# Kernel tuning notes

Measured on AMD Instinct MI355X. Metric: run time of the kernel, lower is better.

## Reference

```python
import jax, jax.numpy as jnp
import numpy as np

B, CIN, F, H, W = 4, 256, 128, 64, 64
EPS = 1e-5

def _conv1x1(x, Wm, b):
    # x: [B,C,H,W], Wm: [O,C] (1x1 conv kernel), b: [O]
    return jnp.einsum('bchw,oc->bohw', x, Wm) + b[None, :, None, None]

def setup_inputs() -> dict:
    key = jax.random.key(0)
    ks = jax.random.split(key, 11)
    s_in = 1.0 / np.sqrt(CIN)
    s_f = 1.0 / np.sqrt(F)
    return {
        'x':    jax.random.normal(ks[0], (B, CIN, H, W), jnp.float32),
        'Wg':   jax.random.normal(ks[1], (F, CIN), jnp.float32) * s_in,
        'bg':   jax.random.normal(ks[2], (F,), jnp.float32) * s_in,
        'Wt':   jax.random.normal(ks[3], (F, CIN), jnp.float32) * s_in,
        'bt':   jax.random.normal(ks[4], (F,), jnp.float32) * s_in,
        'Wp':   jax.random.normal(ks[5], (F, CIN), jnp.float32) * s_in,
        'bp':   jax.random.normal(ks[6], (F,), jnp.float32) * s_in,
        'Wz':   jax.random.normal(ks[7], (CIN, F), jnp.float32) * s_f,
        'bz':   jax.random.normal(ks[8], (CIN,), jnp.float32) * s_f,
        'ln_w': jax.random.normal(ks[9], (CIN, H, W), jnp.float32) * 0.1,
        'ln_b': jax.random.normal(ks[10], (CIN, H, W), jnp.float32) * 0.1,
    }

def reference(x, Wg, bg, Wt, bt, Wp, bp, Wz, bz, ln_w, ln_b):
    b, _, h, w = x.shape
    n = h * w
    # 1x1 conv projections
    g = _conv1x1(x, Wg, bg).reshape(b, F, n).transpose(0, 2, 1)      # [B,N,F]
    theta = _conv1x1(x, Wt, bt).reshape(b, F, n).transpose(0, 2, 1)  # [B,N,F]
    phi = _conv1x1(x, Wp, bp).reshape(b, F, n)                        # [B,F,N]
    # embedded-Gaussian affinity + softmax attention
    f = jnp.einsum('bnf,bfm->bnm', theta, phi)                        # [B,N,N]
    attn = jax.nn.softmax(f, axis=-1)
    y = jnp.einsum('bnm,bmf->bnf', attn, g)                           # [B,N,F]
    y = y.transpose(0, 2, 1).reshape(b, F, h, w)                      # [B,F,H,W]
    # output projection
    z = _conv1x1(y, Wz, bz)                                           # [B,CIN,H,W]
    # LayerNorm over (C,H,W) per sample, affine params shaped [C,H,W]
    mu = jnp.mean(z, axis=(1, 2, 3), keepdims=True)
    var = jnp.var(z, axis=(1, 2, 3), keepdims=True)
    z = (z - mu) * jax.lax.rsqrt(var + EPS)
    z = z * ln_w[None] + ln_b[None]
    return z + x
```

## Files before the change

### kernel.cpp

```cpp
#include <hip/hip_runtime.h>
#include <stdint.h>

#define CIN 256
#define FDIM 128
#define NSP 4096
#define EPS 1e-5f

typedef __attribute__((ext_vector_type(8))) short short8;
typedef __attribute__((ext_vector_type(4))) float f32x4;
typedef __attribute__((ext_vector_type(16))) float f32x16;

__device__ __forceinline__ short f2bf(float f) {
  union { float f; uint32_t u; } v; v.f = f;
  uint32_t r = v.u + 0x7fffu + ((v.u >> 16) & 1u);
  return (short)(r >> 16);
}
__device__ __forceinline__ float bf2f(short h) {
  union { uint32_t u; float f; } v; v.u = ((uint32_t)(uint16_t)h) << 16;
  return v.f;
}

__global__ void prep_w(const float* __restrict__ Wg, const float* __restrict__ Wt,
                       const float* __restrict__ Wp, const float* __restrict__ Wz,
                       short* __restrict__ Wbf, short* __restrict__ Wzbf,
                       float* __restrict__ sums) {
  int u = blockIdx.x * 256 + threadIdx.x;
  if (u < 8 && blockIdx.x == 0) sums[u] = 0.f;
  if (u < 12288) {
    int p = u >> 12;
    int rem = u & 4095;
    int ftg = rem >> 9, s = (rem >> 6) & 7, lane = rem & 63;
    int row = ftg * 16 + (lane & 15);
    int col = s * 32 + (lane >> 4) * 8;
    const float* Wsrc = (p == 0) ? Wt : (p == 1) ? Wp : Wg;
    short8 v8;
#pragma unroll
    for (int j = 0; j < 8; j++) v8[j] = f2bf(Wsrc[row * 256 + col + j]);
    *(short8*)(Wbf + (size_t)u * 8) = v8;
  } else if (u < 12288 + 4096) {
    int u2 = u - 12288;
    int cog = u2 >> 8, s = (u2 >> 6) & 3, lane = u2 & 63;
    int co = cog * 16 + (lane & 15);
    int ch = s * 32 + (lane >> 4) * 8;
    short8 v8;
#pragma unroll
    for (int j = 0; j < 8; j++) v8[j] = f2bf(Wz[co * 128 + ch + j]);
    *(short8*)(Wzbf + (size_t)u2 * 8) = v8;
  }
}

__global__ void __launch_bounds__(256)
proj_kernel(const float* __restrict__ x, const short* __restrict__ Wbf,
            const float* __restrict__ bt, const float* __restrict__ bp,
            const float* __restrict__ bg,
            short* __restrict__ theta, short* __restrict__ Kb, short* __restrict__ gT) {
  __shared__ float tile[32][33];
  __shared__ short Axy[32 * 264];
  __shared__ short lds[5120];
  int bx = blockIdx.x;
  int b = bx >> 7;
  int n0 = (bx & 127) << 5;
  int t = threadIdx.x, w = t >> 6, lane = t & 63, l15 = lane & 15, quad = lane >> 4;
  int r = t >> 5, cc = t & 31;

  const float* xb = x + (size_t)b * CIN * NSP;
#pragma unroll
  for (int ch = 0; ch < 8; ch++) {
    int c0 = ch * 32;
#pragma unroll
    for (int k = 0; k < 4; k++)
      tile[r + 8 * k][cc] = xb[(size_t)(c0 + r + 8 * k) * NSP + n0 + cc];
    __syncthreads();
#pragma unroll
    for (int k = 0; k < 4; k++)
      Axy[(r + 8 * k) * 264 + c0 + cc] = f2bf(tile[cc][r + 8 * k]);
    __syncthreads();
  }

  short8 a[8];
  int ar = (w & 1) * 16 + l15;
#pragma unroll
  for (int s = 0; s < 8; s++)
    a[s] = *(const short8*)(Axy + ar * 264 + s * 32 + quad * 8);

  for (int p = 0; p < 3; p++) {
    const short* Wsrc = Wbf + p * 32768;
    f32x4 zero = {0.f, 0.f, 0.f, 0.f};
    f32x4 acc[4];
#pragma unroll
    for (int i = 0; i < 4; i++) acc[i] = zero;

#pragma unroll
    for (int s = 0; s < 8; s++) {
#pragma unroll
      for (int ft = 0; ft < 4; ft++) {
        int ftg = (w >> 1) * 4 + ft;
        short8 bfr = *(const short8*)(Wsrc + (ftg * 8 + s) * 512 + lane * 8);
        acc[ft] = __builtin_amdgcn_mfma_f32_16x16x32_bf16(a[s], bfr, acc[ft], 0, 0, 0);
      }
    }

    const float* bias = (p == 0) ? bt : (p == 1) ? bp : bg;
    if (p > 0) __syncthreads();
    if (p < 2) {
#pragma unroll
      for (int ft = 0; ft < 4; ft++) {
        int ftg = (w >> 1) * 4 + ft;
        float bv = bias[ftg * 16 + l15];
#pragma unroll
        for (int rr = 0; rr < 4; rr++) {
          int n = (w & 1) * 16 + quad * 4 + rr;
          lds[n * 136 + ftg * 16 + l15] = f2bf(acc[ft][rr] + bv);
        }
      }
      __syncthreads();
      short* dst = ((p == 0) ? theta : Kb) + (size_t)(b * NSP + n0) * FDIM;
#pragma unroll
      for (int i = 0; i < 2; i++) {
        int flat = t + 256 * i;
        int row = flat >> 4, ch = flat & 15;
        *(short8*)(dst + (size_t)row * FDIM + ch * 8) = *(const short8*)(lds + row * 136 + ch * 8);
      }
    } else {
#pragma unroll
      for (int ft = 0; ft < 4; ft++) {
        int ftg = (w >> 1) * 4 + ft;
        float bv = bias[ftg * 16 + l15];
#pragma unroll
        for (int rr = 0; rr < 4; rr++) {
          int n = (w & 1) * 16 + quad * 4 + rr;
          lds[(ftg * 16 + l15) * 40 + n] = f2bf(acc[ft][rr] + bv);
        }
      }
      __syncthreads();
      short* dst = gT + (size_t)b * FDIM * NSP + n0;
#pragma unroll
      for (int i = 0; i < 2; i++) {
        int flat = t + 256 * i;
        int f = flat >> 2, c = flat & 3;
        *(short8*)(dst + (size_t)f * NSP + c * 8) = *(const short8*)(lds + f * 40 + c * 8);
      }
    }
  }
}

__global__ void __launch_bounds__(256, 2)
flash_kernel(const short* __restrict__ thetab, const short* __restrict__ Kb,
             const short* __restrict__ gT, short* __restrict__ opart,
             float* __restrict__ lpart) {
  __shared__ __attribute__((aligned(16))) char smem[34816];
  short* Klds = (short*)smem;
  short* Vlds = (short*)(smem + 16384);

  const int bx = blockIdx.x;
  const int b  = bx >> 7;
  const int r  = bx & 127;
  const int q0 = (r >> 2) << 7;
  const int kc = r & 3;
  const int t = threadIdx.x, w = t >> 6, lane = t & 63;
  const int l31 = lane & 31, h = lane >> 5;
  const int qw = q0 + w * 32;

  const short* Qsrc = thetab + (size_t)b * NSP * FDIM;
  const short* Ksrc = Kb + (size_t)b * NSP * FDIM;
  const short* Vsrc = gT + (size_t)b * FDIM * NSP;

  short8 qf[8];
#pragma unroll
  for (int s = 0; s < 8; s++)
    qf[s] = *(const short8*)(Qsrc + (size_t)(qw + l31) * FDIM + s * 16 + h * 8);

  f32x16 O[4];
#pragma unroll
  for (int i = 0; i < 4; i++)
#pragma unroll
    for (int j = 0; j < 16; j++) O[i][j] = 0.f;
  float lsum = 0.f;

  const int kr0 = t >> 4, kcc0 = t & 15, kr1 = kr0 + 16;
  const int woK0 = kcc0 * 256 + ((kr0 ^ (kcc0 & 7)) * 8);
  const int woK1 = kcc0 * 256 + ((kr1 ^ (kcc0 & 7)) * 8);
  const int vf0 = t >> 2, vcc0 = t & 3, vf1 = 64 + (t >> 2);
  const int woV0 = vcc0 * 1024 + ((vf0 ^ (vcc0 & 3)) * 8);
  const int woV1 = vcc0 * 1024 + ((vf1 ^ (vcc0 & 3)) * 8);

  const int kA0 = kc << 10;
  short8 rKa0, rKa1, rKb0, rKb1, rVa0, rVa1, rVb0, rVb1;

  {
    rKa0 = *(const short8*)(Ksrc + (size_t)(kA0 + kr0) * FDIM + kcc0 * 8);
    rKa1 = *(const short8*)(Ksrc + (size_t)(kA0 + kr1) * FDIM + kcc0 * 8);
    rKb0 = *(const short8*)(Ksrc + (size_t)(kA0 + 32 + kr0) * FDIM + kcc0 * 8);
    rKb1 = *(const short8*)(Ksrc + (size_t)(kA0 + 32 + kr1) * FDIM + kcc0 * 8);
    rVa0 = *(const short8*)(Vsrc + (size_t)vf0 * NSP + kA0 + vcc0 * 8);
    rVa1 = *(const short8*)(Vsrc + (size_t)vf1 * NSP + kA0 + vcc0 * 8);
    rVb0 = *(const short8*)(Vsrc + (size_t)vf0 * NSP + kA0 + 32 + vcc0 * 8);
    rVb1 = *(const short8*)(Vsrc + (size_t)vf1 * NSP + kA0 + 32 + vcc0 * 8);
    *(short8*)(Klds + woK0) = rKa0;
    *(short8*)(Klds + woK1) = rKa1;
    *(short8*)(Klds + 4096 + woK0) = rKb0;
    *(short8*)(Klds + 4096 + woK1) = rKb1;
    *(short8*)(Vlds + woV0) = rVa0;
    *(short8*)(Vlds + woV1) = rVa1;
    *(short8*)(Vlds + 4096 + woV0) = rVb0;
    *(short8*)(Vlds + 4096 + woV1) = rVb1;
  }

#pragma unroll 2
  for (int it = 0; it < 16; ++it) {
    __syncthreads();
    if (it < 15) {
      int kn = kA0 + (it + 1) * 64;
      rKa0 = *(const short8*)(Ksrc + (size_t)(kn + kr0) * FDIM + kcc0 * 8);
      rKa1 = *(const short8*)(Ksrc + (size_t)(kn + kr1) * FDIM + kcc0 * 8);
      rKb0 = *(const short8*)(Ksrc + (size_t)(kn + 32 + kr0) * FDIM + kcc0 * 8);
      rKb1 = *(const short8*)(Ksrc + (size_t)(kn + 32 + kr1) * FDIM + kcc0 * 8);
      rVa0 = *(const short8*)(Vsrc + (size_t)vf0 * NSP + kn + vcc0 * 8);
      rVa1 = *(const short8*)(Vsrc + (size_t)vf1 * NSP + kn + vcc0 * 8);
      rVb0 = *(const short8*)(Vsrc + (size_t)vf0 * NSP + kn + 32 + vcc0 * 8);
      rVb1 = *(const short8*)(Vsrc + (size_t)vf1 * NSP + kn + 32 + vcc0 * 8);
    }

    f32x16 S0, S1;
#pragma unroll
    for (int j = 0; j < 16; j++) { S0[j] = 0.f; S1[j] = 0.f; }
    __builtin_amdgcn_s_setprio(1);
#pragma unroll
    for (int s = 0; s < 8; s++) {
      int c = 2 * s + h;
      const short* base = Klds + c * 256 + ((l31 ^ (c & 7)) * 8);
      short8 ak0 = *(const short8*)(base);
      short8 ak1 = *(const short8*)(base + 4096);
      S0 = __builtin_amdgcn_mfma_f32_32x32x16_bf16(ak0, qf[s], S0, 0, 0, 0);
      S1 = __builtin_amdgcn_mfma_f32_32x32x16_bf16(ak1, qf[s], S1, 0, 0, 0);
    }
    __builtin_amdgcn_s_setprio(0);

    short8 AfA[2], AfB[2];
#pragma unroll
    for (int sub = 0; sub < 2; sub++) {
      float p[16];
#pragma unroll
      for (int i = 0; i < 16; i++) p[i] = __expf(sub ? S1[i] : S0[i]);
      float t8[8];
#pragma unroll
      for (int i = 0; i < 8; i++) t8[i] = p[2 * i] + p[2 * i + 1];
      lsum += ((t8[0] + t8[1]) + (t8[2] + t8[3])) + ((t8[4] + t8[5]) + (t8[6] + t8[7]));

      uint32_t W[8];
#pragma unroll
      for (int j = 0; j < 8; j++)
        asm("v_cvt_pk_bf16_f32 %0, %1, %2" : "=v"(W[j]) : "v"(p[2 * j]), "v"(p[2 * j + 1]));
      asm("v_permlane32_swap_b32 %0, %1" : "+v"(W[0]), "+v"(W[2]));
      asm("v_permlane32_swap_b32 %0, %1" : "+v"(W[1]), "+v"(W[3]));
      asm("v_permlane32_swap_b32 %0, %1" : "+v"(W[4]), "+v"(W[6]));
      asm("v_permlane32_swap_b32 %0, %1" : "+v"(W[5]), "+v"(W[7]));
      union { short8 s; uint32_t u[4]; } u0, u1;
      u0.u[0] = W[0]; u0.u[1] = W[1]; u0.u[2] = W[2]; u0.u[3] = W[3];
      u1.u[0] = W[4]; u1.u[1] = W[5]; u1.u[2] = W[6]; u1.u[3] = W[7];
      if (sub) { AfB[0] = u0.s; AfB[1] = u1.s; }
      else     { AfA[0] = u0.s; AfA[1] = u1.s; }
    }

    __builtin_amdgcn_s_setprio(1);
#pragma unroll
    for (int ft = 0; ft < 4; ft++) {
#pragma unroll
      for (int tt = 0; tt < 2; tt++) {
        int c = tt * 2 + h;
        int off = c * 1024 + ft * 256 + ((l31 ^ (c & 3)) * 8);
        short8 bva = *(const short8*)(Vlds + off);
        O[ft] = __builtin_amdgcn_mfma_f32_32x32x16_bf16(AfA[tt], bva, O[ft], 0, 0, 0);
        short8 bvb = *(const short8*)(Vlds + off + 4096);
        O[ft] = __builtin_amdgcn_mfma_f32_32x32x16_bf16(AfB[tt], bvb, O[ft], 0, 0, 0);
      }
    }
    __builtin_amdgcn_s_setprio(0);

    __syncthreads();
    if (it < 15) {
      *(short8*)(Klds + woK0) = rKa0;
      *(short8*)(Klds + woK1) = rKa1;
      *(short8*)(Klds + 4096 + woK0) = rKb0;
      *(short8*)(Klds + 4096 + woK1) = rKb1;
      *(short8*)(Vlds + woV0) = rVa0;
      *(short8*)(Vlds + woV1) = rVa1;
      *(short8*)(Vlds + 4096 + woV0) = rVb0;
      *(short8*)(Vlds + 4096 + woV1) = rVb1;
    }
  }

  lsum += __shfl_xor(lsum, 32, 64);

  short* tr = (short*)smem + w * 32 * 136;
#pragma unroll
  for (int ft = 0; ft < 4; ft++) {
#pragma unroll
    for (int reg = 0; reg < 16; reg++) {
      int rowq = (reg & 3) + 8 * (reg >> 2) + 4 * h;
      tr[rowq * 136 + ft * 32 + l31] = f2bf(O[ft][reg]);
    }
  }
  short* od = opart + ((size_t)(kc * 4 + b) * NSP + qw) * FDIM;
#pragma unroll
  for (int i = 0; i < 8; i++) {
    int slot = lane + 64 * i;
    int row = slot >> 4, c = slot & 15;
    *(short8*)(od + (size_t)row * FDIM + c * 8) = *(const short8*)(tr + row * 136 + c * 8);
  }
  if (h == 0) lpart[(size_t)(kc * 4 + b) * NSP + qw + l31] = lsum;
}

__global__ void __launch_bounds__(256)
zproj_kernel(const short* __restrict__ opart, const float* __restrict__ lpart,
             const short* __restrict__ Wzbf, const float* __restrict__ bz,
             short* __restrict__ zb, float* __restrict__ sums) {
  __shared__ short Alds[32 * 136];
  __shared__ short ldsT[128 * 40];
  __shared__ float Linv[32];
  __shared__ float wsum[4][2];
  int bx = blockIdx.x;
  int b = bx >> 7;
  int n0 = (bx & 127) << 5;
  int ch0 = blockIdx.y * 128;
  int t = threadIdx.x, w = t >> 6, lane = t & 63, l15 = lane & 15, quad = lane >> 4;

  if (t < 32) {
    float L = 0.f;
#pragma unroll
    for (int kcc = 0; kcc < 4; kcc++) L += lpart[(size_t)(kcc * 4 + b) * NSP + n0 + t];
    Linv[t] = 1.0f / L;
  }
  __syncthreads();

#pragma unroll
  for (int iter = 0; iter < 2; iter++) {
    int i = t + 256 * iter;
    int row = i >> 4, c16 = i & 15;
    const short* base = opart + ((size_t)b * NSP + n0 + row) * FDIM + c16 * 8;
    float accv[8] = {0, 0, 0, 0, 0, 0, 0, 0};
#pragma unroll
    for (int kcc = 0; kcc < 4; kcc++) {
      short8 v = *(const short8*)(base + (size_t)kcc * 4 * NSP * FDIM);
#pragma unroll
      for (int j = 0; j < 8; j++) accv[j] += bf2f(v[j]);
    }
    float inv = Linv[row];
    short8 av;
#pragma unroll
    for (int j = 0; j < 8; j++) av[j] = f2bf(accv[j] * inv);
    *(short8*)(Alds + row * 136 + c16 * 8) = av;
  }
  __syncthreads();

  short8 a[4];
#pragma unroll
  for (int s = 0; s < 4; s++)
    a[s] = *(const short8*)(Alds + ((w & 1) * 16 + l15) * 136 + s * 32 + quad * 8);

  f32x4 zero = {0.f, 0.f, 0.f, 0.f};
  f32x4 acc[4];
#pragma unroll
  for (int i = 0; i < 4; i++) acc[i] = zero;
#pragma unroll
  for (int s = 0; s < 4; s++) {
#pragma unroll
    for (int ct = 0; ct < 4; ct++) {
      int cog = blockIdx.y * 8 + (w >> 1) * 4 + ct;
      short8 bfr = *(const short8*)(Wzbf + cog * 2048 + s * 512 + lane * 8);
      acc[ct] = __builtin_amdgcn_mfma_f32_16x16x32_bf16(a[s], bfr, acc[ct], 0, 0, 0);
    }
  }

  float s1 = 0.0f, s2 = 0.0f;
#pragma unroll
  for (int ct = 0; ct < 4; ct++) {
    int cg = (w >> 1) * 64 + ct * 16 + l15;
    float bv = bz[ch0 + cg];
#pragma unroll
    for (int rr = 0; rr < 4; rr++) {
      float v = acc[ct][rr] + bv;
      s1 += v; s2 += v * v;
      ldsT[cg * 40 + (w & 1) * 16 + quad * 4 + rr] = f2bf(v);
    }
  }
#pragma unroll
  for (int off = 32; off >= 1; off >>= 1) {
    s1 += __shfl_xor(s1, off, 64);
    s2 += __shfl_xor(s2, off, 64);
  }
  if (lane == 0) { wsum[w][0] = s1; wsum[w][1] = s2; }
  __syncthreads();
  if (t == 0) {
    atomicAdd(&sums[b * 2],     wsum[0][0] + wsum[1][0] + wsum[2][0] + wsum[3][0]);
    atomicAdd(&sums[b * 2 + 1], wsum[0][1] + wsum[1][1] + wsum[2][1] + wsum[3][1]);
  }
  short* dst = zb + (size_t)b * CIN * NSP + (size_t)ch0 * NSP + n0;
#pragma unroll
  for (int i = 0; i < 2; i++) {
    int flat = t + 256 * i;
    int c = flat >> 2, ch = flat & 3;
    *(short8*)(dst + (size_t)c * NSP + ch * 8) = *(const short8*)(ldsT + c * 40 + ch * 8);
  }
}

__global__ void __launch_bounds__(256)
finalize_kernel(const short* __restrict__ zbuf, const float* __restrict__ x,
                const float* __restrict__ lnw, const float* __restrict__ lnb,
                const float* __restrict__ sums, float* __restrict__ out) {
  int gid = blockIdx.x * 256 + threadIdx.x;
  size_t e0 = (size_t)gid * 8;
  int b = (int)(e0 >> 20);
  size_t ib = e0 & ((size_t)(1u << 20) - 1);
  float mean = sums[b * 2] * (1.0f / 1048576.0f);
  float var = sums[b * 2 + 1] * (1.0f / 1048576.0f) - mean * mean;
  float rs = rsqrtf(var + EPS);
  short8 zv = *(const short8*)(zbuf + e0);
  f32x4 xv0 = *(const f32x4*)(x + e0),   xv1 = *(const f32x4*)(x + e0 + 4);
  f32x4 wv0 = *(const f32x4*)(lnw + ib), wv1 = *(const f32x4*)(lnw + ib + 4);
  f32x4 bv0 = *(const f32x4*)(lnb + ib), bv1 = *(const f32x4*)(lnb + ib + 4);
  f32x4 o0, o1;
#pragma unroll
  for (int k = 0; k < 4; k++) {
    o0[k] = (bf2f(zv[k]) - mean) * rs * wv0[k] + bv0[k] + xv0[k];
    o1[k] = (bf2f(zv[k + 4]) - mean) * rs * wv1[k] + bv1[k] + xv1[k];
  }
  *(f32x4*)(out + e0) = o0;
  *(f32x4*)(out + e0 + 4) = o1;
}

extern "C" void kernel_launch(void* const* d_in, const int* in_sizes, int n_in,
                              void* d_out, int out_size, void* d_ws, size_t ws_size,
                              hipStream_t stream) {
  const float* x   = (const float*)d_in[0];
  const float* Wg  = (const float*)d_in[1];
  const float* bg  = (const float*)d_in[2];
  const float* Wt  = (const float*)d_in[3];
  const float* bt  = (const float*)d_in[4];
  const float* Wp  = (const float*)d_in[5];
  const float* bp  = (const float*)d_in[6];
  const float* Wz  = (const float*)d_in[7];
  const float* bz  = (const float*)d_in[8];
  const float* lnw = (const float*)d_in[9];
  const float* lnb = (const float*)d_in[10];
  float* out = (float*)d_out;

  char* ws = (char*)d_ws;
  short* Wbf    = (short*)(ws);
  short* Wzbf   = (short*)(ws + 196608);
  short* opart  = (short*)(ws + 262144);
  float* lpart  = (float*)(ws + 17039360);
  short* thetab = (short*)(ws + 17301504);
  short* Kb     = (short*)(ws + 21495808);
  short* gT     = (short*)(ws + 25690112);
  short* zb     = (short*)(ws + 17301504);
  float* sums   = (float*)(ws + 29884416);

  prep_w<<<64, 256, 0, stream>>>(Wg, Wt, Wp, Wz, Wbf, Wzbf, sums);
  proj_kernel<<<512, 256, 0, stream>>>(x, Wbf, bt, bp, bg, thetab, Kb, gT);
  flash_kernel<<<512, 256, 0, stream>>>(thetab, Kb, gT, opart, lpart);
  zproj_kernel<<<dim3(512, 2), 256, 0, stream>>>(opart, lpart, Wzbf, bz, zb, sums);
  finalize_kernel<<<2048, 256, 0, stream>>>(zb, x, lnw, lnb, sums, out);
}
```

Before: 180.5 us.

## Double per-wave query tile in flash kernel to reuse K/V fragments

Each wave now processes 64 query rows, as two 32-row MFMA chains, instead of 32. This lets every K and V fragment read from LDS feed two MFMAs, aiming to halve LDS read traffic per unit of compute. The grid halves to 256 blocks and launch bounds drop to one block per SM. The cost is double the accumulator registers and fewer resident waves to hide latency.

```diff
diff --git a/kernel.cpp b/kernel.cpp
--- a/kernel.cpp
+++ b/kernel.cpp
@@ -144,7 +144,7 @@
   }
 }
 
-__global__ void __launch_bounds__(256, 2)
+__global__ void __launch_bounds__(256, 1)
 flash_kernel(const short* __restrict__ thetab, const short* __restrict__ Kb,
              const short* __restrict__ gT, short* __restrict__ opart,
              float* __restrict__ lpart) {
@@ -153,29 +153,31 @@
   short* Vlds = (short*)(smem + 16384);
 
   const int bx = blockIdx.x;
-  const int b  = bx >> 7;
-  const int r  = bx & 127;
-  const int q0 = (r >> 2) << 7;
+  const int b  = bx >> 6;
+  const int r  = bx & 63;
+  const int q0 = (r >> 2) << 8;
   const int kc = r & 3;
   const int t = threadIdx.x, w = t >> 6, lane = t & 63;
   const int l31 = lane & 31, h = lane >> 5;
-  const int qw = q0 + w * 32;
+  const int qw = q0 + w * 64;
 
   const short* Qsrc = thetab + (size_t)b * NSP * FDIM;
   const short* Ksrc = Kb + (size_t)b * NSP * FDIM;
   const short* Vsrc = gT + (size_t)b * FDIM * NSP;
 
-  short8 qf[8];
-#pragma unroll
-  for (int s = 0; s < 8; s++)
-    qf[s] = *(const short8*)(Qsrc + (size_t)(qw + l31) * FDIM + s * 16 + h * 8);
-
-  f32x16 O[4];
+  short8 qf0[8], qf1[8];
+#pragma unroll
+  for (int s = 0; s < 8; s++) {
+    qf0[s] = *(const short8*)(Qsrc + (size_t)(qw + l31) * FDIM + s * 16 + h * 8);
+    qf1[s] = *(const short8*)(Qsrc + (size_t)(qw + 32 + l31) * FDIM + s * 16 + h * 8);
+  }
+
+  f32x16 O0[4], O1[4];
 #pragma unroll
   for (int i = 0; i < 4; i++)
 #pragma unroll
-    for (int j = 0; j < 16; j++) O[i][j] = 0.f;
-  float lsum = 0.f;
+    for (int j = 0; j < 16; j++) { O0[i][j] = 0.f; O1[i][j] = 0.f; }
+  float lsum0 = 0.f, lsum1 = 0.f;
 
   const int kr0 = t >> 4, kcc0 = t & 15, kr1 = kr0 + 16;
   const int woK0 = kcc0 * 256 + ((kr0 ^ (kcc0 & 7)) * 8);
@@ -221,31 +223,35 @@
       rVb1 = *(const short8*)(Vsrc + (size_t)vf1 * NSP + kn + 32 + vcc0 * 8);
     }
 
-    f32x16 S0, S1;
-#pragma unroll
-    for (int j = 0; j < 16; j++) { S0[j] = 0.f; S1[j] = 0.f; }
+    f32x16 SA0, SA1, SB0, SB1;
+#pragma unroll
+    for (int j = 0; j < 16; j++) { SA0[j] = 0.f; SA1[j] = 0.f; SB0[j] = 0.f; SB1[j] = 0.f; }
     __builtin_amdgcn_s_setprio(1);
 #pragma unroll
     for (int s = 0; s < 8; s++) {
       int c = 2 * s + h;
       const short* base = Klds + c * 256 + ((l31 ^ (c & 7)) * 8);
-      short8 ak0 = *(const short8*)(base);
-      short8 ak1 = *(const short8*)(base + 4096);
-      S0 = __builtin_amdgcn_mfma_f32_32x32x16_bf16(ak0, qf[s], S0, 0, 0, 0);
-      S1 = __builtin_amdgcn_mfma_f32_32x32x16_bf16(ak1, qf[s], S1, 0, 0, 0);
+      short8 akA = *(const short8*)(base);
+      short8 akB = *(const short8*)(base + 4096);
+      SA0 = __builtin_amdgcn_mfma_f32_32x32x16_bf16(akA, qf0[s], SA0, 0, 0, 0);
+      SA1 = __builtin_amdgcn_mfma_f32_32x32x16_bf16(akA, qf1[s], SA1, 0, 0, 0);
+      SB0 = __builtin_amdgcn_mfma_f32_32x32x16_bf16(akB, qf0[s], SB0, 0, 0, 0);
+      SB1 = __builtin_amdgcn_mfma_f32_32x32x16_bf16(akB, qf1[s], SB1, 0, 0, 0);
     }
     __builtin_amdgcn_s_setprio(0);
 
-    short8 AfA[2], AfB[2];
-#pragma unroll
-    for (int sub = 0; sub < 2; sub++) {
+    short8 AfA0[2], AfA1[2], AfB0[2], AfB1[2];
+#pragma unroll
+    for (int chain = 0; chain < 4; chain++) {
       float p[16];
 #pragma unroll
-      for (int i = 0; i < 16; i++) p[i] = __expf(sub ? S1[i] : S0[i]);
+      for (int i = 0; i < 16; i++)
+        p[i] = __expf(chain == 0 ? SA0[i] : chain == 1 ? SA1[i] : chain == 2 ? SB0[i] : SB1[i]);
       float t8[8];
 #pragma unroll
       for (int i = 0; i < 8; i++) t8[i] = p[2 * i] + p[2 * i + 1];
-      lsum += ((t8[0] + t8[1]) + (t8[2] + t8[3])) + ((t8[4] + t8[5]) + (t8[6] + t8[7]));
+      float ls = ((t8[0] + t8[1]) + (t8[2] + t8[3])) + ((t8[4] + t8[5]) + (t8[6] + t8[7]));
+      if (chain & 1) lsum1 += ls; else lsum0 += ls;
 
       uint32_t W[8];
 #pragma unroll
@@ -258,8 +264,10 @@
       union { short8 s; uint32_t u[4]; } u0, u1;
       u0.u[0] = W[0]; u0.u[1] = W[1]; u0.u[2] = W[2]; u0.u[3] = W[3];
       u1.u[0] = W[4]; u1.u[1] = W[5]; u1.u[2] = W[6]; u1.u[3] = W[7];
-      if (sub) { AfB[0] = u0.s; AfB[1] = u1.s; }
-      else     { AfA[0] = u0.s; AfA[1] = u1.s; }
+      if (chain == 0)      { AfA0[0] = u0.s; AfA0[1] = u1.s; }
+      else if (chain == 1) { AfA1[0] = u0.s; AfA1[1] = u1.s; }
+      else if (chain == 2) { AfB0[0] = u0.s; AfB0[1] = u1.s; }
+      else                 { AfB1[0] = u0.s; AfB1[1] = u1.s; }
     }
 
     __builtin_amdgcn_s_setprio(1);
@@ -269,10 +277,12 @@
       for (int tt = 0; tt < 2; tt++) {
         int c = tt * 2 + h;
         int off = c * 1024 + ft * 256 + ((l31 ^ (c & 3)) * 8);
-        short8 bva = *(const short8*)(Vlds + off);
-        O[ft] = __builtin_amdgcn_mfma_f32_32x32x16_bf16(AfA[tt], bva, O[ft], 0, 0, 0);
-        short8 bvb = *(const short8*)(Vlds + off + 4096);
-        O[ft] = __builtin_amdgcn_mfma_f32_32x32x16_bf16(AfB[tt], bvb, O[ft], 0, 0, 0);
+        short8 bvA = *(const short8*)(Vlds + off);
+        O0[ft] = __builtin_amdgcn_mfma_f32_32x32x16_bf16(AfA0[tt], bvA, O0[ft], 0, 0, 0);
+        O1[ft] = __builtin_amdgcn_mfma_f32_32x32x16_bf16(AfA1[tt], bvA, O1[ft], 0, 0, 0);
+        short8 bvB = *(const short8*)(Vlds + off + 4096);
+        O0[ft] = __builtin_amdgcn_mfma_f32_32x32x16_bf16(AfB0[tt], bvB, O0[ft], 0, 0, 0);
+        O1[ft] = __builtin_amdgcn_mfma_f32_32x32x16_bf16(AfB1[tt], bvB, O1[ft], 0, 0, 0);
       }
     }
     __builtin_amdgcn_s_setprio(0);
@@ -290,25 +300,34 @@
     }
   }
 
-  lsum += __shfl_xor(lsum, 32, 64);
+  lsum0 += __shfl_xor(lsum0, 32, 64);
+  lsum1 += __shfl_xor(lsum1, 32, 64);
 
   short* tr = (short*)smem + w * 32 * 136;
 #pragma unroll
-  for (int ft = 0; ft < 4; ft++) {
-#pragma unroll
-    for (int reg = 0; reg < 16; reg++) {
-      int rowq = (reg & 3) + 8 * (reg >> 2) + 4 * h;
-      tr[rowq * 136 + ft * 32 + l31] = f2bf(O[ft][reg]);
-    }
-  }
-  short* od = opart + ((size_t)(kc * 4 + b) * NSP + qw) * FDIM;
-#pragma unroll
-  for (int i = 0; i < 8; i++) {
-    int slot = lane + 64 * i;
-    int row = slot >> 4, c = slot & 15;
-    *(short8*)(od + (size_t)row * FDIM + c * 8) = *(const short8*)(tr + row * 136 + c * 8);
-  }
-  if (h == 0) lpart[(size_t)(kc * 4 + b) * NSP + qw + l31] = lsum;
+  for (int qb = 0; qb < 2; qb++) {
+#pragma unroll
+    for (int ft = 0; ft < 4; ft++) {
+#pragma unroll
+      for (int reg = 0; reg < 16; reg++) {
+        int rowq = (reg & 3) + 8 * (reg >> 2) + 4 * h;
+        float v = qb ? O1[ft][reg] : O0[ft][reg];
+        tr[rowq * 136 + ft * 32 + l31] = f2bf(v);
+      }
+    }
+    short* od = opart + ((size_t)(kc * 4 + b) * NSP + qw + qb * 32) * FDIM;
+#pragma unroll
+    for (int i = 0; i < 8; i++) {
+      int slot = lane + 64 * i;
+      int row = slot >> 4, c = slot & 15;
+      *(short8*)(od + (size_t)row * FDIM + c * 8) = *(const short8*)(tr + row * 136 + c * 8);
+    }
+  }
+  if (h == 0) {
+    size_t lb = (size_t)(kc * 4 + b) * NSP + qw;
+    lpart[lb + l31] = lsum0;
+    lpart[lb + 32 + l31] = lsum1;
+  }
 }
 
 __global__ void __launch_bounds__(256)
@@ -458,7 +477,7 @@
 
   prep_w<<<64, 256, 0, stream>>>(Wg, Wt, Wp, Wz, Wbf, Wzbf, sums);
   proj_kernel<<<512, 256, 0, stream>>>(x, Wbf, bt, bp, bg, thetab, Kb, gT);
-  flash_kernel<<<512, 256, 0, stream>>>(thetab, Kb, gT, opart, lpart);
+  flash_kernel<<<256, 256, 0, stream>>>(thetab, Kb, gT, opart, lpart);
   zproj_kernel<<<dim3(512, 2), 256, 0, stream>>>(opart, lpart, Wzbf, bz, zb, sums);
   finalize_kernel<<<2048, 256, 0, stream>>>(zb, x, lnw, lnb, sums, out);
 }
```

Measured after the change: 190.2 us. 1.05x slower.

## Double-buffer x tile load in projection and interleave attention split partials

Applied to the files above, without the earlier changes.

The projection kernel now prefetches the next 32-channel slab of x into registers while the current slab is transposed from a double-buffered shared tile, removing one barrier per iteration and overlapping global loads with the transpose. The attention partial outputs and row sums are also re-laid out so that the four key-chunk partials for each query are contiguous. This lets the z-projection kernel read them with nearby loads and a single vector load for the sums. It costs extra registers and shared memory in the projection kernel, and the attention kernel's writes become strided.

```diff
diff --git a/kernel.cpp b/kernel.cpp
--- a/kernel.cpp
+++ b/kernel.cpp
@@ -54,7 +54,7 @@
             const float* __restrict__ bt, const float* __restrict__ bp,
             const float* __restrict__ bg,
             short* __restrict__ theta, short* __restrict__ Kb, short* __restrict__ gT) {
-  __shared__ float tile[32][33];
+  __shared__ float tile[2][32][33];
   __shared__ short Axy[32 * 264];
   __shared__ short lds[5120];
   int bx = blockIdx.x;
@@ -64,18 +64,29 @@
   int r = t >> 5, cc = t & 31;
 
   const float* xb = x + (size_t)b * CIN * NSP;
+  float rv[4];
+#pragma unroll
+  for (int k = 0; k < 4; k++) rv[k] = xb[(size_t)(r + 8 * k) * NSP + n0 + cc];
+#pragma unroll
+  for (int k = 0; k < 4; k++) tile[0][r + 8 * k][cc] = rv[k];
+
 #pragma unroll
   for (int ch = 0; ch < 8; ch++) {
-    int c0 = ch * 32;
+    __syncthreads();
+    if (ch < 7) {
+      int c0 = (ch + 1) * 32;
+#pragma unroll
+      for (int k = 0; k < 4; k++) rv[k] = xb[(size_t)(c0 + r + 8 * k) * NSP + n0 + cc];
+    }
 #pragma unroll
     for (int k = 0; k < 4; k++)
-      tile[r + 8 * k][cc] = xb[(size_t)(c0 + r + 8 * k) * NSP + n0 + cc];
-    __syncthreads();
-#pragma unroll
-    for (int k = 0; k < 4; k++)
-      Axy[(r + 8 * k) * 264 + c0 + cc] = f2bf(tile[cc][r + 8 * k]);
-    __syncthreads();
-  }
+      Axy[(r + 8 * k) * 264 + ch * 32 + cc] = f2bf(tile[ch & 1][cc][r + 8 * k]);
+    if (ch < 7) {
+#pragma unroll
+      for (int k = 0; k < 4; k++) tile[(ch + 1) & 1][r + 8 * k][cc] = rv[k];
+    }
+  }
+  __syncthreads();
 
   short8 a[8];
   int ar = (w & 1) * 16 + l15;
@@ -301,14 +312,14 @@
       tr[rowq * 136 + ft * 32 + l31] = f2bf(O[ft][reg]);
     }
   }
-  short* od = opart + ((size_t)(kc * 4 + b) * NSP + qw) * FDIM;
+  short* od = opart + ((size_t)(b * NSP + qw) * 4 + kc) * FDIM;
 #pragma unroll
   for (int i = 0; i < 8; i++) {
     int slot = lane + 64 * i;
     int row = slot >> 4, c = slot & 15;
-    *(short8*)(od + (size_t)row * FDIM + c * 8) = *(const short8*)(tr + row * 136 + c * 8);
-  }
-  if (h == 0) lpart[(size_t)(kc * 4 + b) * NSP + qw + l31] = lsum;
+    *(short8*)(od + (size_t)row * 4 * FDIM + c * 8) = *(const short8*)(tr + row * 136 + c * 8);
+  }
+  if (h == 0) lpart[((size_t)b * NSP + qw + l31) * 4 + kc] = lsum;
 }
 
 __global__ void __launch_bounds__(256)
@@ -326,10 +337,8 @@
   int t = threadIdx.x, w = t >> 6, lane = t & 63, l15 = lane & 15, quad = lane >> 4;
 
   if (t < 32) {
-    float L = 0.f;
-#pragma unroll
-    for (int kcc = 0; kcc < 4; kcc++) L += lpart[(size_t)(kcc * 4 + b) * NSP + n0 + t];
-    Linv[t] = 1.0f / L;
+    f32x4 L4 = *(const f32x4*)(lpart + ((size_t)b * NSP + n0 + t) * 4);
+    Linv[t] = 1.0f / ((L4[0] + L4[1]) + (L4[2] + L4[3]));
   }
   __syncthreads();
 
@@ -337,11 +346,11 @@
   for (int iter = 0; iter < 2; iter++) {
     int i = t + 256 * iter;
     int row = i >> 4, c16 = i & 15;
-    const short* base = opart + ((size_t)b * NSP + n0 + row) * FDIM + c16 * 8;
+    const short* base = opart + ((size_t)(b * NSP + n0 + row) * 4) * FDIM + c16 * 8;
     float accv[8] = {0, 0, 0, 0, 0, 0, 0, 0};
 #pragma unroll
     for (int kcc = 0; kcc < 4; kcc++) {
-      short8 v = *(const short8*)(base + (size_t)kcc * 4 * NSP * FDIM);
+      short8 v = *(const short8*)(base + kcc * FDIM);
 #pragma unroll
       for (int j = 0; j < 8; j++) accv[j] += bf2f(v[j]);
     }
```

Measured after the change: 194.8 us. 1.08x slower.
